# Optimization experiments

Measured on AMD Instinct MI355X. Metric: run time of the kernel, lower is better.

The kernel has to match this reference:

```python
import jax, jax.numpy as jnp
import numpy as np
from jax import lax

NVOX = 100
EPS = 1e-4
DN = ('NDHWC', 'DHWIO', 'NDHWC')

# scn semantics emulated densely: inactive voxels are identically zero and the
# active-site mask is re-applied after every layer, so submanifold convolution,
# strided sparse conv, sparse deconv and masked BN-ReLU compute the same values
# at active sites as SparseConvNet's rulebook gather-GEMM-scatter.

def _bnrelu(x, p, mask):
    # p: [4, C] = (gamma, beta, running_mean, running_var); inference-form BN.
    g, b, mu, v = p[0], p[1], p[2], p[3]
    return jax.nn.relu((x - mu) * (g * lax.rsqrt(v + EPS)) + b) * mask

def _subconv(x, w, mask):
    # Submanifold conv: inputs outside active set are zero; outputs only at active sites.
    return lax.conv_general_dilated(x, w, (1, 1, 1), 'SAME', dimension_numbers=DN) * mask

def _down(x, w):
    # scn.Convolution(dim, a, b, size=2, stride=2, bias=False)
    return lax.conv_general_dilated(x, w, (2, 2, 2), 'VALID', dimension_numbers=DN)

def _up(x, w, mask):
    # scn.Deconvolution restores the pre-downsample active set -> mask with finer mask.
    return lax.conv_transpose(x, w, (2, 2, 2), 'VALID', dimension_numbers=DN) * mask

def _pool_mask(mask):
    return lax.reduce_window(mask, 0.0, lax.max, (1, 2, 2, 2, 1), (1, 2, 2, 2, 1), 'VALID')

def _forward(coords, feats, w_in, w0a, wdown0, w1a, wdown1, w2, wup1, w1post, wup0, w0post,
             bnA, bnB, bnC, bnD, bnE, bnF, bnG, bnH, bnI, bnJ, linW, linb):
    i, j, k = coords[:, 0], coords[:, 1], coords[:, 2]
    # InputLayer mode=3: sum features at duplicate coordinates.
    grid = jnp.zeros((1, NVOX, NVOX, NVOX, 1), feats.dtype).at[0, i, j, k, 0].add(feats[:, 0])
    mask0 = jnp.zeros((1, NVOX, NVOX, NVOX, 1), feats.dtype).at[0, i, j, k, 0].set(1.0)
    mask1 = _pool_mask(mask0)   # 50^3 active set after strided conv
    mask2 = _pool_mask(mask1)   # 25^3

    x = _subconv(grid, w_in, mask0)                          # 1 -> 32
    x0 = _subconv(_bnrelu(x, bnA, mask0), w0a, mask0)        # level-0 VGG block
    d0 = _down(_bnrelu(x0, bnB, mask0), wdown0)              # 32 -> 64, 100 -> 50
    x1 = _subconv(_bnrelu(d0, bnC, mask1), w1a, mask1)       # level-1 VGG block
    d1 = _down(_bnrelu(x1, bnD, mask1), wdown1)              # 64 -> 96, 50 -> 25
    x2 = _subconv(_bnrelu(d1, bnE, mask2), w2, mask2)        # level-2 VGG block
    u1 = _up(_bnrelu(x2, bnF, mask2), wup1, mask1)           # 96 -> 64, 25 -> 50
    y1 = _subconv(_bnrelu(jnp.concatenate([x1, u1], -1), bnG, mask1), w1post, mask1)  # 128 -> 64
    u0 = _up(_bnrelu(y1, bnH, mask1), wup0, mask0)           # 64 -> 32, 50 -> 100
    y0 = _subconv(_bnrelu(jnp.concatenate([x0, u0], -1), bnI, mask0), w0post, mask0)  # 64 -> 32
    y = _bnrelu(y0, bnJ, mask0)                              # final BatchNormReLU(32)
    pts = y[0, i, j, k, :]                                   # OutputLayer: gather active sites [N,32]
    return pts @ linW + linb                                 # Linear(32, 3)


def setup_inputs() -> dict:
    key = jax.random.key(0)
    ks = jax.random.split(key, 24)
    N = 120000
    coords = jax.random.randint(ks[0], (N, 3), 0, NVOX, dtype=jnp.int32)
    feats = jax.random.normal(ks[1], (N, 1), jnp.float32)

    def w(k, shape, fan_in):
        return (jax.random.normal(k, shape, jnp.float32) / np.float32(np.sqrt(fan_in)))

    def bn(k, c):
        k1, k2, k3, k4 = jax.random.split(k, 4)
        return jnp.stack([
            1.0 + 0.1 * jax.random.normal(k1, (c,)),
            0.1 * jax.random.normal(k2, (c,)),
            0.1 * jax.random.normal(k3, (c,)),
            0.5 + jax.random.uniform(k4, (c,)),
        ]).astype(jnp.float32)

    return dict(
        coords=coords, feats=feats,
        w_in=w(ks[2], (3, 3, 3, 1, 32), 27),
        w0a=w(ks[3], (3, 3, 3, 32, 32), 27 * 32),
        wdown0=w(ks[4], (2, 2, 2, 32, 64), 8 * 32),
        w1a=w(ks[5], (3, 3, 3, 64, 64), 27 * 64),
        wdown1=w(ks[6], (2, 2, 2, 64, 96), 8 * 64),
        w2=w(ks[7], (3, 3, 3, 96, 96), 27 * 96),
        wup1=w(ks[8], (2, 2, 2, 96, 64), 96),
        w1post=w(ks[9], (3, 3, 3, 128, 64), 27 * 128),
        wup0=w(ks[10], (2, 2, 2, 64, 32), 64),
        w0post=w(ks[11], (3, 3, 3, 64, 32), 27 * 64),
        bnA=bn(ks[12], 32), bnB=bn(ks[13], 32), bnC=bn(ks[14], 64), bnD=bn(ks[15], 64),
        bnE=bn(ks[16], 96), bnF=bn(ks[17], 96), bnG=bn(ks[18], 128), bnH=bn(ks[19], 64),
        bnI=bn(ks[20], 64), bnJ=bn(ks[21], 32),
        linW=w(ks[22], (32, 3), 32),
        linb=0.01 * jax.random.normal(ks[23], (3,), jnp.float32),
    )


def reference(coords, feats, w_in, w0a, wdown0, w1a, wdown1, w2, wup1, w1post, wup0, w0post,
              bnA, bnB, bnC, bnD, bnE, bnF, bnG, bnH, bnI, bnJ, linW, linb):
    return _forward(coords, feats, w_in, w0a, wdown0, w1a, wdown1, w2, wup1, w1post, wup0, w0post,
                    bnA, bnB, bnC, bnD, bnE, bnF, bnG, bnH, bnI, bnJ, linW, linb)
```

## Files before the change

kernel.cpp:

```cpp
#include <hip/hip_runtime.h>


#define NVOX 100
#define EPSB 1e-4f
typedef unsigned long long u64;
typedef _Float16 h2 __attribute__((ext_vector_type(2)));
typedef _Float16 h8 __attribute__((ext_vector_type(8)));
typedef float f16v __attribute__((ext_vector_type(16)));
#define DEVFN __device__ __forceinline__

DEVFN float bnr(float v, float sc, float sh) { return fmaxf(fmaf(v, sc, sh), 0.f); }

template<int NTAPS, int CTOT, int COUT>
__global__ __launch_bounds__(256)
void prepB32(const float* __restrict__ w, h2* __restrict__ out)
{
    constexpr int CTG = COUT / 32, KCH = CTOT / 16;
    const int n = NTAPS * CTG * KCH * 256;
    const int idx = blockIdx.x * 256 + threadIdx.x;
    if (idx >= n) return;
    const int jh = idx & 3;
    const int lane = (idx >> 2) & 63;
    int r = idx >> 8;
    const int kc = r % KCH; r /= KCH;
    const int ct = r % CTG; const int t = r / CTG;
    const int k0 = kc * 16 + (lane >> 5) * 8 + 2 * jh;
    const int co = ct * 32 + (lane & 31);
    h2 v;
    v[0] = (_Float16)w[((size_t)t * CTOT + k0) * COUT + co];
    v[1] = (_Float16)w[((size_t)t * CTOT + k0 + 1) * COUT + co];
    out[idx] = v;
}

template<int EMODE, int COUT>
DEVFN void epilogue(float a, int srow, int ch,
                    float* outF, _Float16* o1, const float* sc1, const float* sh1,
                    _Float16* o2, const float* sc2, const float* sh2)
{
    if constexpr (EMODE == 0) {
        outF[(size_t)srow * COUT + ch] = a;
    } else if constexpr (EMODE == 3) {
        outF[(size_t)srow * COUT + ch] = bnr(a, sc1[ch], sh1[ch]);
    } else {
        o1[(size_t)srow * COUT + ch] = (_Float16)bnr(a, sc1[ch], sh1[ch]);
        if constexpr (EMODE == 2)
            o2[(size_t)srow * COUT + ch] = (_Float16)bnr(a, sc2[ch], sh2[ch]);
    }
}

template<int KC1, int KC2, int COUT, int S, int EMODE>
__global__ __launch_bounds__(64)
void gconv_m32(const h2* __restrict__ inA, const h2* __restrict__ inB,
               const h2* __restrict__ wb,
               const int* __restrict__ amap, const int* __restrict__ vlist,
               const int* __restrict__ cnt, int cap,
               float* __restrict__ outF, _Float16* __restrict__ o1,
               const float* __restrict__ sc1, const float* __restrict__ sh1,
               _Float16* __restrict__ o2,
               const float* __restrict__ sc2, const float* __restrict__ sh2)
{
    constexpr int KCH = KC1 + KC2;
    constexpr int CTG = COUT / 32;
    const int lane = threadIdx.x;
    const int cntv = *cnt;
    const int wbase = blockIdx.x * 32;
    if (wbase >= cntv) return;
    const int ct0 = blockIdx.y;
    const int l31 = lane & 31, ksub = lane >> 5;
    const int slot = wbase + l31;
    const bool on = slot < cntv;
    int X = 0, Y = 0, Z = 0;
    if (on) { const int v = vlist[slot]; X = v % S; const int r = v / S; Y = r % S; Z = r / S; }

    auto calc_ns = [&](int t) -> int {
        int ns = cap;
        if (on) {
            const int dz = t / 9 - 1, dy = (t / 3) % 3 - 1, dx = t % 3 - 1;
            const int nz = Z + dz, ny = Y + dy, nx = X + dx;
            if ((unsigned)nz < (unsigned)S && (unsigned)ny < (unsigned)S &&
                (unsigned)nx < (unsigned)S) {
                const int m = amap[(nz * S + ny) * S + nx];
                if (m >= 0) ns = m;
            }
        }
        return ns;
    };

    f16v acc = (f16v)(0.f);
    int ns = calc_ns(0);
#pragma unroll 1
    for (int t = 0; t < 27; ++t) {
        const int ns_nxt = (t + 1 < 27) ? calc_ns(t + 1) : cap;
        const h2* __restrict__ wt = wb + ((size_t)t * CTG + ct0) * KCH * 256;
#pragma unroll
        for (int kc = 0; kc < KC1; ++kc) {
            const h8 a = *reinterpret_cast<const h8*>(
                inA + (size_t)ns * (KC1 * 8) + kc * 8 + ksub * 4);
            const h8 b = *reinterpret_cast<const h8*>(
                wt + (size_t)kc * 256 + lane * 4);
            acc = __builtin_amdgcn_mfma_f32_32x32x16_f16(a, b, acc, 0, 0, 0);
        }
        if constexpr (KC2 > 0) {
#pragma unroll
            for (int kc = 0; kc < KC2; ++kc) {
                const h8 a = *reinterpret_cast<const h8*>(
                    inB + (size_t)ns * (KC2 * 8) + kc * 8 + ksub * 4);
                const h8 b = *reinterpret_cast<const h8*>(
                    wt + (size_t)(KC1 + kc) * 256 + lane * 4);
                acc = __builtin_amdgcn_mfma_f32_32x32x16_f16(a, b, acc, 0, 0, 0);
            }
        }
        ns = ns_nxt;
    }
    const int ch = ct0 * 32 + l31;
#pragma unroll
    for (int r = 0; r < 16; ++r) {
        const int row = (r & 3) + 8 * (r >> 2) + 4 * ksub;
        const int srow = wbase + row;
        if (srow < cntv)
            epilogue<EMODE, COUT>(acc[r], srow, ch, outF, o1, sc1, sh1, o2, sc2, sh2);
    }
}

template<int KCH, int COUT, int SC, int EMODE>
__global__ __launch_bounds__(64)
void dconv_m32(const h2* __restrict__ in, const h2* __restrict__ wb,
               const int* __restrict__ amap_f, const int* __restrict__ vlist_c,
               const int* __restrict__ cnt_c, int capf,
               float* __restrict__ outF, _Float16* __restrict__ o1,
               const float* __restrict__ sc1, const float* __restrict__ sh1)
{
    constexpr int SF = SC * 2;
    constexpr int CTG = COUT / 32;
    const int lane = threadIdx.x;
    const int cntv = *cnt_c;
    const int wbase = blockIdx.x * 32;
    if (wbase >= cntv) return;
    const int ct0 = blockIdx.y;
    const int l31 = lane & 31, ksub = lane >> 5;
    const int slot = wbase + l31;
    const bool on = slot < cntv;
    int X = 0, Y = 0, Z = 0;
    if (on) { const int v = vlist_c[slot]; X = v % SC; const int r = v / SC; Y = r % SC; Z = r / SC; }

    auto calc_ns = [&](int t) -> int {
        int ns = capf;
        if (on) {
            const int fz = 2 * Z + ((t >> 2) & 1);
            const int fy = 2 * Y + ((t >> 1) & 1);
            const int fx = 2 * X + (t & 1);
            const int m = amap_f[(fz * SF + fy) * SF + fx];
            if (m >= 0) ns = m;
        }
        return ns;
    };

    f16v acc = (f16v)(0.f);
    int ns = calc_ns(0);
#pragma unroll 1
    for (int t = 0; t < 8; ++t) {
        const int ns_nxt = (t + 1 < 8) ? calc_ns(t + 1) : capf;
        const h2* __restrict__ wt = wb + ((size_t)t * CTG + ct0) * KCH * 256;
#pragma unroll
        for (int kc = 0; kc < KCH; ++kc) {
            const h8 a = *reinterpret_cast<const h8*>(
                in + (size_t)ns * (KCH * 8) + kc * 8 + ksub * 4);
            const h8 b = *reinterpret_cast<const h8*>(
                wt + (size_t)kc * 256 + lane * 4);
            acc = __builtin_amdgcn_mfma_f32_32x32x16_f16(a, b, acc, 0, 0, 0);
        }
        ns = ns_nxt;
    }
    const int ch = ct0 * 32 + l31;
#pragma unroll
    for (int r = 0; r < 16; ++r) {
        const int row = (r & 3) + 8 * (r >> 2) + 4 * ksub;
        const int srow = wbase + row;
        if (srow < cntv)
            epilogue<EMODE, COUT>(acc[r], srow, ch, outF, o1, sc1, sh1,
                                  nullptr, nullptr, nullptr);
    }
}


template<int CTOT, int COUT>
DEVFN void stage_tap(const float* __restrict__ wtap, int cg32,
                     float* __restrict__ lbuf, int wid, int lane)
{
    constexpr int IPW = CTOT / 32;
#pragma unroll
    for (int i = 0; i < IPW; ++i) {
        const int chunk = wid * IPW + i;
        const int f4i = chunk * 64 + lane;
        const int ci = f4i >> 3, sub = f4i & 7;
        const float* g = wtap + ci * COUT + cg32 + sub * 4;
        __builtin_amdgcn_global_load_lds(
            (const __attribute__((address_space(1))) void*)g,
            (__attribute__((address_space(3))) void*)(lbuf + chunk * 256),
            16, 0, 0);
    }
}

template<int CIN>
DEVFN void dorow8(const float* __restrict__ row, const float* __restrict__ wl,
                  float (&acc)[8])
{
#pragma unroll 4
    for (int c0 = 0; c0 < CIN; c0 += 4) {
        const float4 a = *reinterpret_cast<const float4*>(row + c0);
        const float av[4] = {a.x, a.y, a.z, a.w};
#pragma unroll
        for (int j = 0; j < 4; ++j) {
            const float4 w0 = *reinterpret_cast<const float4*>(wl + (c0 + j) * 32);
            const float4 w1 = *reinterpret_cast<const float4*>(wl + (c0 + j) * 32 + 4);
            acc[0] = fmaf(av[j], w0.x, acc[0]);
            acc[1] = fmaf(av[j], w0.y, acc[1]);
            acc[2] = fmaf(av[j], w0.z, acc[2]);
            acc[3] = fmaf(av[j], w0.w, acc[3]);
            acc[4] = fmaf(av[j], w1.x, acc[4]);
            acc[5] = fmaf(av[j], w1.y, acc[5]);
            acc[6] = fmaf(av[j], w1.z, acc[6]);
            acc[7] = fmaf(av[j], w1.w, acc[7]);
        }
    }
}

template<int CIN, int COUT, int SC>
__global__ __launch_bounds__(256)
void uconv_w(const float* __restrict__ in, const float* __restrict__ w,
             const int* __restrict__ amap_f, const int* __restrict__ vlist_c,
             const int* __restrict__ cnt_c, _Float16* __restrict__ out,
             const float* __restrict__ sc, const float* __restrict__ sh)
{
    constexpr int SF = SC * 2;
    __shared__ float lw[2][CIN * 32];
    const int tid = threadIdx.x, lane = tid & 63, wid = tid >> 6;
    const int cntv = *cnt_c;
    if (blockIdx.x * 64 >= cntv) return;
    const int slot = blockIdx.x * 64 + lane;
    const int cg32 = blockIdx.y * 32;
    const bool on = slot < cntv;
    int X = 0, Y = 0, Z = 0;
    if (on) { const int v = vlist_c[slot]; X = v % SC; const int r = v / SC; Y = r % SC; Z = r / SC; }
    stage_tap<CIN, COUT>(w + (size_t)7 * CIN * COUT, cg32, lw[0], wid, lane);
    __syncthreads();
#pragma unroll 1
    for (int t = 0; t < 8; ++t) {
        if (t + 1 < 8)
            stage_tap<CIN, COUT>(w + (size_t)(6 - t) * CIN * COUT, cg32,
                                 lw[(t + 1) & 1], wid, lane);
        int cs = -1;
        if (on) {
            const int fz = 2 * Z + ((t >> 2) & 1);
            const int fy = 2 * Y + ((t >> 1) & 1);
            const int fx = 2 * X + (t & 1);
            cs = amap_f[(fz * SF + fy) * SF + fx];
        }
        if (cs >= 0) {
            float acc[8];
#pragma unroll
            for (int q = 0; q < 8; ++q) acc[q] = 0.f;
            dorow8<CIN>(in + (size_t)slot * CIN, &lw[t & 1][wid * 8], acc);
            union { float4 v[1]; _Float16 h[8]; } o;
            const int chb = cg32 + wid * 8;
#pragma unroll
            for (int q = 0; q < 8; ++q)
                o.h[q] = (_Float16)bnr(acc[q], sc[chb + q], sh[chb + q]);
            *reinterpret_cast<float4*>(out + (size_t)cs * COUT + chb) = o.v[0];
        }
        __syncthreads();
    }
}

template<int S>
__global__ __launch_bounds__(128)
void cin_k(const float* __restrict__ grid, const float* __restrict__ w,
           const int* __restrict__ vlist, const int* __restrict__ cnt,
           _Float16* __restrict__ out, const float* __restrict__ sc,
           const float* __restrict__ sh)
{
    const int wOff = __builtin_amdgcn_readfirstlane(threadIdx.x >> 6) * 16;
    const int slot = blockIdx.x * 64 + (threadIdx.x & 63);
    if (slot >= *cnt) return;
    const int v = vlist[slot];
    const int x = v % S;
    const int rem = v / S;
    const int y = rem % S;
    const int z = rem / S;
    float acc[16];
#pragma unroll
    for (int c = 0; c < 16; ++c) acc[c] = 0.f;
#pragma unroll
    for (int t = 0; t < 27; ++t) {
        const int dz = t / 9 - 1, dy = (t / 3) % 3 - 1, dx = t % 3 - 1;
        const int nz = z + dz, ny = y + dy, nx = x + dx;
        if ((unsigned)nz >= (unsigned)S || (unsigned)ny >= (unsigned)S ||
            (unsigned)nx >= (unsigned)S) continue;
        const float val = grid[(nz * S + ny) * S + nx];
        const float* __restrict__ wp = w + t * 32 + wOff;
#pragma unroll
        for (int c = 0; c < 16; ++c) acc[c] = fmaf(val, wp[c], acc[c]);
    }
    union { float4 v[2]; _Float16 h[16]; } o;
#pragma unroll
    for (int c = 0; c < 16; ++c)
        o.h[c] = (_Float16)bnr(acc[c], sc[wOff + c], sh[wOff + c]);
    float4* dst = reinterpret_cast<float4*>(out + (size_t)slot * 32 + wOff);
    dst[0] = o.v[0];
    dst[1] = o.v[1];
}

__global__ __launch_bounds__(256)
void final_k(const int* __restrict__ coords, const float* __restrict__ y0,
             const int* __restrict__ amap0, const float* __restrict__ ssJ,
             const float* __restrict__ linW, const float* __restrict__ linb,
             int N, float* __restrict__ outp)
{
    const int n = blockIdx.x * blockDim.x + threadIdx.x;
    if (n >= N) return;
    const int i = coords[3 * n + 0];
    const int j = coords[3 * n + 1];
    const int k = coords[3 * n + 2];
    const int v = (i * NVOX + j) * NVOX + k;
    const int s = amap0[v];
    float a0 = linb[0], a1 = linb[1], a2 = linb[2];
    if (s >= 0) {
        const float* __restrict__ row = y0 + (size_t)s * 32;
#pragma unroll
        for (int c = 0; c < 32; ++c) {
            const float t = bnr(row[c], ssJ[c], ssJ[32 + c]);
            a0 = fmaf(t, linW[c * 3 + 0], a0);
            a1 = fmaf(t, linW[c * 3 + 1], a1);
            a2 = fmaf(t, linW[c * 3 + 2], a2);
        }
    }
    outp[3 * n + 0] = a0;
    outp[3 * n + 1] = a1;
    outp[3 * n + 2] = a2;
}

__global__ void bn_prep(const float* __restrict__ A, const float* __restrict__ B,
                        const float* __restrict__ C, const float* __restrict__ D,
                        const float* __restrict__ E, const float* __restrict__ F,
                        const float* __restrict__ G, const float* __restrict__ H,
                        const float* __restrict__ I, const float* __restrict__ J,
                        float* __restrict__ ss)
{
    const float* bp[10] = {A, B, C, D, E, F, G, H, I, J};
    const int CH[10] = {32, 32, 64, 64, 96, 96, 128, 64, 64, 32};
    int idx = blockIdx.x * blockDim.x + threadIdx.x;
    if (idx >= 672) return;
    int l = 0, base = 0, off2 = 0;
    while (idx >= base + CH[l]) { base += CH[l]; off2 += 2 * CH[l]; ++l; }
    const int c = idx - base;
    const float* bn = bp[l];
    const int Cc = CH[l];
    const float g = bn[c], b = bn[Cc + c], mu = bn[2 * Cc + c], var = bn[3 * Cc + c];
    const float sc = g * rsqrtf(var + EPSB);
    ss[off2 + c] = sc;
    ss[off2 + Cc + c] = b - mu * sc;
}

__global__ __launch_bounds__(256)
void scatter_mark(const int* __restrict__ coords, const float* __restrict__ feats,
                  int N, float* __restrict__ grid, int* __restrict__ amap0)
{
    const int n = blockIdx.x * blockDim.x + threadIdx.x;
    if (n >= N) return;
    const int i = coords[3 * n + 0];
    const int j = coords[3 * n + 1];
    const int k = coords[3 * n + 2];
    const int v = (i * NVOX + j) * NVOX + k;
    atomicAdd(&grid[v], feats[n]);
    amap0[v] = -2;
}

template<int SC>
__global__ __launch_bounds__(256)
void flag_coarse(const int* __restrict__ amap_f, int* __restrict__ amap_c)
{
    constexpr int SF = SC * 2;
    const int v = blockIdx.x * blockDim.x + threadIdx.x;
    if (v >= SC * SC * SC) return;
    const int x = v % SC;
    const int rem = v / SC;
    const int y = rem % SC;
    const int z = rem / SC;
    bool any = false;
#pragma unroll
    for (int t = 0; t < 8; ++t) {
        const int fz = 2 * z + ((t >> 2) & 1);
        const int fy = 2 * y + ((t >> 1) & 1);
        const int fx = 2 * x + (t & 1);
        if (amap_f[(fz * SF + fy) * SF + fx] >= 0) any = true;
    }
    amap_c[v] = any ? -2 : -1;
}

__global__ __launch_bounds__(256)
void count_k(const int* __restrict__ flags, int V, int* __restrict__ counts)
{
    const int v = blockIdx.x * 256 + threadIdx.x;
    const bool act = (v < V) && (flags[v] == -2);
    const u64 m = __ballot(act);
    __shared__ int c[4];
    const int wid = threadIdx.x >> 6;
    if ((threadIdx.x & 63) == 0) c[wid] = __popcll(m);
    __syncthreads();
    if (threadIdx.x == 0) counts[blockIdx.x] = c[0] + c[1] + c[2] + c[3];
}

__global__ __launch_bounds__(1024)
void scan_k(int* __restrict__ counts, int nb, int* __restrict__ total)
{
    __shared__ int sums[1024];
    const int t = threadIdx.x;
    int v[4];
    int s = 0;
#pragma unroll
    for (int i = 0; i < 4; ++i) {
        const int idx = t * 4 + i;
        v[i] = (idx < nb) ? counts[idx] : 0;
        s += v[i];
    }
    sums[t] = s;
    __syncthreads();
    for (int d = 1; d < 1024; d <<= 1) {
        const int add = (t >= d) ? sums[t - d] : 0;
        __syncthreads();
        sums[t] += add;
        __syncthreads();
    }
    int base = (t > 0) ? sums[t - 1] : 0;
#pragma unroll
    for (int i = 0; i < 4; ++i) {
        const int idx = t * 4 + i;
        if (idx < nb) counts[idx] = base;
        base += v[i];
    }
    if (t == 1023) *total = sums[1023];
}

__global__ __launch_bounds__(256)
void emit_k(int* __restrict__ amap, int V, const int* __restrict__ offsets,
            int* __restrict__ vlist)
{
    const int v = blockIdx.x * 256 + threadIdx.x;
    const bool act = (v < V) && (amap[v] == -2);
    const u64 m = __ballot(act);
    __shared__ int wbase[4];
    const int wid = threadIdx.x >> 6;
    const int lane = threadIdx.x & 63;
    if (lane == 0) wbase[wid] = __popcll(m);
    __syncthreads();
    if (threadIdx.x == 0) {
        int s = 0;
#pragma unroll
        for (int i = 0; i < 4; ++i) { const int t = wbase[i]; wbase[i] = s; s += t; }
    }
    __syncthreads();
    if (act) {
        const int slot = offsets[blockIdx.x] + wbase[wid] +
                         __popcll(m & ((1ull << lane) - 1ull));
        amap[v] = slot;
        vlist[slot] = v;
    }
}

extern "C" void kernel_launch(void* const* d_in, const int* in_sizes, int n_in,
                              void* d_out, int out_size, void* d_ws, size_t ws_size,
                              hipStream_t stream) {
    const int*   coords = (const int*)d_in[0];
    const float* feats  = (const float*)d_in[1];
    const float* w_in   = (const float*)d_in[2];
    const float* w0a    = (const float*)d_in[3];
    const float* wdown0 = (const float*)d_in[4];
    const float* w1a    = (const float*)d_in[5];
    const float* wdown1 = (const float*)d_in[6];
    const float* w2     = (const float*)d_in[7];
    const float* wup1   = (const float*)d_in[8];
    const float* w1post = (const float*)d_in[9];
    const float* wup0   = (const float*)d_in[10];
    const float* w0post = (const float*)d_in[11];
    const float* linW = (const float*)d_in[22];
    const float* linb = (const float*)d_in[23];
    float* outp = (float*)d_out;

    const int N = in_sizes[1];
    const int V0 = NVOX * NVOX * NVOX;
    const int V1 = 50 * 50 * 50;
    const int V2 = 25 * 25 * 25;
    const int cap0 = N;
    const int cap1 = 100000;
    const int cap2 = V2;

    char* ws = (char*)d_ws;
    size_t off = 0;
    auto alloc = [&](size_t bytes) -> void* {
        void* p = ws + off;
        off += (bytes + 255) & ~(size_t)255;
        return p;
    };
    int*   amap0  = (int*)alloc((size_t)V0 * 4);
    int*   vlist0 = (int*)alloc((size_t)cap0 * 4);
    int*   amap1  = (int*)alloc((size_t)V1 * 4);
    int*   vlist1 = (int*)alloc((size_t)cap1 * 4);
    int*   amap2  = (int*)alloc((size_t)V2 * 4);
    int*   vlist2 = (int*)alloc((size_t)cap2 * 4);
    int*   cnt    = (int*)alloc(3 * 4);
    int*   counts = (int*)alloc(4096 * 4);
    float* ss     = (float*)alloc(1344 * 4);
    float* grid   = (float*)alloc((size_t)V0 * 4);
    _Float16* HA  = (_Float16*)alloc((size_t)(cap0 + 1) * 32 * 2);
    _Float16* HB  = (_Float16*)alloc((size_t)(cap0 + 1) * 32 * 2);
    _Float16* HI1 = (_Float16*)alloc((size_t)(cap0 + 1) * 32 * 2);
    _Float16* HI2 = (_Float16*)alloc((size_t)(cap0 + 1) * 32 * 2);
    _Float16* HC  = (_Float16*)alloc((size_t)(cap1 + 1) * 64 * 2);
    _Float16* HD  = (_Float16*)alloc((size_t)(cap1 + 1) * 64 * 2);
    _Float16* HG1 = (_Float16*)alloc((size_t)(cap1 + 1) * 64 * 2);
    _Float16* HG2 = (_Float16*)alloc((size_t)(cap1 + 1) * 64 * 2);
    _Float16* HE  = (_Float16*)alloc((size_t)(cap2 + 1) * 96 * 2);
    float* y0f  = (float*)alloc((size_t)cap0 * 32 * 4);
    float* actF = (float*)alloc((size_t)cap2 * 96 * 4);
    float* actH = (float*)alloc((size_t)cap1 * 64 * 4);
    h2* wbA  = (h2*)alloc((size_t)27 * 1 * 2 * 256 * 4);
    h2* wb1  = (h2*)alloc((size_t)27 * 2 * 4 * 256 * 4);
    h2* wb2  = (h2*)alloc((size_t)27 * 3 * 6 * 256 * 4);
    h2* wbP1 = (h2*)alloc((size_t)27 * 2 * 8 * 256 * 4);
    h2* wbP0 = (h2*)alloc((size_t)27 * 1 * 4 * 256 * 4);
    h2* wbD0 = (h2*)alloc((size_t)8 * 2 * 2 * 256 * 4);
    h2* wbD1 = (h2*)alloc((size_t)8 * 3 * 4 * 256 * 4);
    if (off > ws_size) return;

    const int B = 256;
    const int gN  = (N + B - 1) / B;
    const int nb0 = (V0 + B - 1) / B;
    const int nb1 = (V1 + B - 1) / B;
    const int nb2 = (V2 + B - 1) / B;
    const int sb0 = (cap0 + 63) / 64;
    const int sb1 = (cap1 + 63) / 64;
    const int sb2 = (cap2 + 63) / 64;
    const int g1w_0 = (cap0 + 31) / 32;
    const int g1w_1 = (cap1 + 31) / 32;
    const int g1w_2 = (cap2 + 31) / 32;

    hipMemsetAsync(amap0, 0xFF, (size_t)V0 * 4, stream);
    hipMemsetAsync(grid, 0, (size_t)V0 * 4, stream);
    hipMemsetAsync(HA + (size_t)cap0 * 32, 0, 64, stream);
    hipMemsetAsync(HB + (size_t)cap0 * 32, 0, 64, stream);
    hipMemsetAsync(HI1 + (size_t)cap0 * 32, 0, 64, stream);
    hipMemsetAsync(HI2 + (size_t)cap0 * 32, 0, 64, stream);
    hipMemsetAsync(HC + (size_t)cap1 * 64, 0, 128, stream);
    hipMemsetAsync(HD + (size_t)cap1 * 64, 0, 128, stream);
    hipMemsetAsync(HG1 + (size_t)cap1 * 64, 0, 128, stream);
    hipMemsetAsync(HG2 + (size_t)cap1 * 64, 0, 128, stream);
    hipMemsetAsync(HE + (size_t)cap2 * 96, 0, 192, stream);
    bn_prep<<<3, 256, 0, stream>>>((const float*)d_in[12], (const float*)d_in[13],
                                   (const float*)d_in[14], (const float*)d_in[15],
                                   (const float*)d_in[16], (const float*)d_in[17],
                                   (const float*)d_in[18], (const float*)d_in[19],
                                   (const float*)d_in[20], (const float*)d_in[21], ss);
    prepB32<27, 32, 32><<<(27 * 1 * 2 * 256 + 255) / 256, 256, 0, stream>>>(w0a, wbA);
    prepB32<27, 64, 64><<<(27 * 2 * 4 * 256 + 255) / 256, 256, 0, stream>>>(w1a, wb1);
    prepB32<27, 96, 96><<<(27 * 3 * 6 * 256 + 255) / 256, 256, 0, stream>>>(w2, wb2);
    prepB32<27, 128, 64><<<(27 * 2 * 8 * 256 + 255) / 256, 256, 0, stream>>>(w1post, wbP1);
    prepB32<27, 64, 32><<<(27 * 1 * 4 * 256 + 255) / 256, 256, 0, stream>>>(w0post, wbP0);
    prepB32<8, 32, 64><<<(8 * 2 * 2 * 256 + 255) / 256, 256, 0, stream>>>(wdown0, wbD0);
    prepB32<8, 64, 96><<<(8 * 3 * 4 * 256 + 255) / 256, 256, 0, stream>>>(wdown1, wbD1);
    scatter_mark<<<gN, B, 0, stream>>>(coords, feats, N, grid, amap0);
    count_k<<<nb0, B, 0, stream>>>(amap0, V0, counts);
    scan_k<<<1, 1024, 0, stream>>>(counts, nb0, cnt + 0);
    emit_k<<<nb0, B, 0, stream>>>(amap0, V0, counts, vlist0);
    flag_coarse<50><<<nb1, B, 0, stream>>>(amap0, amap1);
    count_k<<<nb1, B, 0, stream>>>(amap1, V1, counts);
    scan_k<<<1, 1024, 0, stream>>>(counts, nb1, cnt + 1);
    emit_k<<<nb1, B, 0, stream>>>(amap1, V1, counts, vlist1);
    flag_coarse<25><<<nb2, B, 0, stream>>>(amap1, amap2);
    count_k<<<nb2, B, 0, stream>>>(amap2, V2, counts);
    scan_k<<<1, 1024, 0, stream>>>(counts, nb2, cnt + 2);
    emit_k<<<nb2, B, 0, stream>>>(amap2, V2, counts, vlist2);

    cin_k<100><<<sb0, 128, 0, stream>>>(grid, w_in, vlist0, cnt + 0, HA,
                                        ss + 0, ss + 32);
    gconv_m32<2, 0, 32, 100, 2><<<dim3(g1w_0, 1), 64, 0, stream>>>(
        (const h2*)HA, nullptr, wbA, amap0, vlist0, cnt + 0, cap0,
        nullptr, HB, ss + 64, ss + 96, HI1, ss + 1152, ss + 1216);
    dconv_m32<2, 64, 50, 1><<<dim3(g1w_1, 2), 64, 0, stream>>>(
        (const h2*)HB, wbD0, amap0, vlist1, cnt + 1, cap0,
        nullptr, HC, ss + 128, ss + 192);
    gconv_m32<4, 0, 64, 50, 2><<<dim3(g1w_1, 2), 64, 0, stream>>>(
        (const h2*)HC, nullptr, wb1, amap1, vlist1, cnt + 1, cap1,
        nullptr, HD, ss + 256, ss + 320, HG1, ss + 768, ss + 896);
    dconv_m32<4, 96, 25, 1><<<dim3(g1w_2, 3), 64, 0, stream>>>(
        (const h2*)HD, wbD1, amap1, vlist2, cnt + 2, cap1,
        nullptr, HE, ss + 384, ss + 480);
    gconv_m32<6, 0, 96, 25, 3><<<dim3(g1w_2, 3), 64, 0, stream>>>(
        (const h2*)HE, nullptr, wb2, amap2, vlist2, cnt + 2, cap2,
        actF, nullptr, ss + 576, ss + 672, nullptr, nullptr, nullptr);
    uconv_w<96, 64, 25><<<dim3(sb2, 2), 256, 0, stream>>>(
        actF, wup1, amap1, vlist2, cnt + 2, HG2, ss + 768 + 64, ss + 896 + 64);
    gconv_m32<4, 4, 64, 50, 3><<<dim3(g1w_1, 2), 64, 0, stream>>>(
        (const h2*)HG1, (const h2*)HG2, wbP1, amap1, vlist1, cnt + 1, cap1,
        actH, nullptr, ss + 1024, ss + 1088, nullptr, nullptr, nullptr);
    uconv_w<64, 32, 50><<<dim3(sb1, 1), 256, 0, stream>>>(
        actH, wup0, amap0, vlist1, cnt + 1, HI2, ss + 1152 + 32, ss + 1216 + 32);
    gconv_m32<2, 2, 32, 100, 0><<<dim3(g1w_0, 1), 64, 0, stream>>>(
        (const h2*)HI1, (const h2*)HI2, wbP0, amap0, vlist0, cnt + 0, cap0,
        y0f, nullptr, nullptr, nullptr, nullptr, nullptr, nullptr);
    final_k<<<gN, B, 0, stream>>>(coords, y0f, amap0, ss + 1280, linW, linb, N, outp);
}
```

Baseline: 552.8 us.

## Compute multiple output-channel tiles per wave and swizzle blocks across XCDs

The gather-GEMM conv kernels gain a CTILES parameter, so one 64-thread wave can compute two 32-channel output tiles at 64-channel levels. Each gathered input fragment is then reused across both tiles instead of being re-gathered by a second block. Launches are flattened to 1D with an XCD-aware block-index remap, so consecutive logical blocks land on the same XCD for L2 locality. The cost is fewer waves and more accumulator registers per wave at the 64-channel levels, which may reduce latency hiding.

```diff
diff --git a/kernel.cpp b/kernel.cpp
--- a/kernel.cpp
+++ b/kernel.cpp
@@ -10,6 +10,13 @@
 #define DEVFN __device__ __forceinline__
 
 DEVFN float bnr(float v, float sc, float sh) { return fmaxf(fmaf(v, sc, sh), 0.f); }
+
+DEVFN int xcd_swz(int orig, int nwg)
+{
+    const int q = nwg >> 3, r = nwg & 7;
+    const int xcd = orig & 7, idx = orig >> 3;
+    return (xcd < r ? xcd * (q + 1) : r * (q + 1) + (xcd - r) * q) + idx;
+}
 
 template<int NTAPS, int CTOT, int COUT>
 __global__ __launch_bounds__(256)
@@ -48,12 +55,12 @@
     }
 }
 
-template<int KC1, int KC2, int COUT, int S, int EMODE>
+template<int KC1, int KC2, int CTILES, int COUT, int S, int EMODE>
 __global__ __launch_bounds__(64)
 void gconv_m32(const h2* __restrict__ inA, const h2* __restrict__ inB,
                const h2* __restrict__ wb,
                const int* __restrict__ amap, const int* __restrict__ vlist,
-               const int* __restrict__ cnt, int cap,
+               const int* __restrict__ cnt, int cap, int nbx,
                float* __restrict__ outF, _Float16* __restrict__ o1,
                const float* __restrict__ sc1, const float* __restrict__ sh1,
                _Float16* __restrict__ o2,
@@ -63,9 +70,10 @@
     constexpr int CTG = COUT / 32;
     const int lane = threadIdx.x;
     const int cntv = *cnt;
-    const int wbase = blockIdx.x * 32;
+    const int sid = xcd_swz(blockIdx.x, gridDim.x);
+    const int ct0 = sid / nbx;
+    const int wbase = (sid - ct0 * nbx) * 32;
     if (wbase >= cntv) return;
-    const int ct0 = blockIdx.y;
     const int l31 = lane & 31, ksub = lane >> 5;
     const int slot = wbase + l31;
     const bool on = slot < cntv;
@@ -86,47 +94,60 @@
         return ns;
     };
 
-    f16v acc = (f16v)(0.f);
+    f16v acc[CTILES];
+#pragma unroll
+    for (int c = 0; c < CTILES; ++c) acc[c] = (f16v)(0.f);
     int ns = calc_ns(0);
 #pragma unroll 1
     for (int t = 0; t < 27; ++t) {
         const int ns_nxt = (t + 1 < 27) ? calc_ns(t + 1) : cap;
-        const h2* __restrict__ wt = wb + ((size_t)t * CTG + ct0) * KCH * 256;
+        const h2* __restrict__ wt =
+            wb + ((size_t)t * CTG + ct0 * CTILES) * KCH * 256;
 #pragma unroll
         for (int kc = 0; kc < KC1; ++kc) {
             const h8 a = *reinterpret_cast<const h8*>(
                 inA + (size_t)ns * (KC1 * 8) + kc * 8 + ksub * 4);
-            const h8 b = *reinterpret_cast<const h8*>(
-                wt + (size_t)kc * 256 + lane * 4);
-            acc = __builtin_amdgcn_mfma_f32_32x32x16_f16(a, b, acc, 0, 0, 0);
+#pragma unroll
+            for (int ct = 0; ct < CTILES; ++ct) {
+                const h8 b = *reinterpret_cast<const h8*>(
+                    wt + ((size_t)ct * KCH + kc) * 256 + lane * 4);
+                acc[ct] = __builtin_amdgcn_mfma_f32_32x32x16_f16(a, b, acc[ct], 0, 0, 0);
+            }
         }
         if constexpr (KC2 > 0) {
 #pragma unroll
             for (int kc = 0; kc < KC2; ++kc) {
                 const h8 a = *reinterpret_cast<const h8*>(
                     inB + (size_t)ns * (KC2 * 8) + kc * 8 + ksub * 4);
-                const h8 b = *reinterpret_cast<const h8*>(
-                    wt + (size_t)(KC1 + kc) * 256 + lane * 4);
-                acc = __builtin_amdgcn_mfma_f32_32x32x16_f16(a, b, acc, 0, 0, 0);
+#pragma unroll
+                for (int ct = 0; ct < CTILES; ++ct) {
+                    const h8 b = *reinterpret_cast<const h8*>(
+                        wt + ((size_t)ct * KCH + KC1 + kc) * 256 + lane * 4);
+                    acc[ct] = __builtin_amdgcn_mfma_f32_32x32x16_f16(a, b, acc[ct], 0, 0, 0);
+                }
             }
         }
         ns = ns_nxt;
     }
-    const int ch = ct0 * 32 + l31;
-#pragma unroll
-    for (int r = 0; r < 16; ++r) {
-        const int row = (r & 3) + 8 * (r >> 2) + 4 * ksub;
-        const int srow = wbase + row;
-        if (srow < cntv)
-            epilogue<EMODE, COUT>(acc[r], srow, ch, outF, o1, sc1, sh1, o2, sc2, sh2);
-    }
-}
-
-template<int KCH, int COUT, int SC, int EMODE>
+#pragma unroll
+    for (int ct = 0; ct < CTILES; ++ct) {
+        const int ch = (ct0 * CTILES + ct) * 32 + l31;
+#pragma unroll
+        for (int r = 0; r < 16; ++r) {
+            const int row = (r & 3) + 8 * (r >> 2) + 4 * ksub;
+            const int srow = wbase + row;
+            if (srow < cntv)
+                epilogue<EMODE, COUT>(acc[ct][r], srow, ch, outF, o1, sc1, sh1,
+                                      o2, sc2, sh2);
+        }
+    }
+}
+
+template<int KCH, int CTILES, int COUT, int SC, int EMODE>
 __global__ __launch_bounds__(64)
 void dconv_m32(const h2* __restrict__ in, const h2* __restrict__ wb,
                const int* __restrict__ amap_f, const int* __restrict__ vlist_c,
-               const int* __restrict__ cnt_c, int capf,
+               const int* __restrict__ cnt_c, int capf, int nbx,
                float* __restrict__ outF, _Float16* __restrict__ o1,
                const float* __restrict__ sc1, const float* __restrict__ sh1)
 {
@@ -134,9 +155,10 @@
     constexpr int CTG = COUT / 32;
     const int lane = threadIdx.x;
     const int cntv = *cnt_c;
-    const int wbase = blockIdx.x * 32;
+    const int sid = xcd_swz(blockIdx.x, gridDim.x);
+    const int ct0 = sid / nbx;
+    const int wbase = (sid - ct0 * nbx) * 32;
     if (wbase >= cntv) return;
-    const int ct0 = blockIdx.y;
     const int l31 = lane & 31, ksub = lane >> 5;
     const int slot = wbase + l31;
     const bool on = slot < cntv;
@@ -155,30 +177,39 @@
         return ns;
     };
 
-    f16v acc = (f16v)(0.f);
+    f16v acc[CTILES];
+#pragma unroll
+    for (int c = 0; c < CTILES; ++c) acc[c] = (f16v)(0.f);
     int ns = calc_ns(0);
 #pragma unroll 1
     for (int t = 0; t < 8; ++t) {
         const int ns_nxt = (t + 1 < 8) ? calc_ns(t + 1) : capf;
-        const h2* __restrict__ wt = wb + ((size_t)t * CTG + ct0) * KCH * 256;
+        const h2* __restrict__ wt =
+            wb + ((size_t)t * CTG + ct0 * CTILES) * KCH * 256;
 #pragma unroll
         for (int kc = 0; kc < KCH; ++kc) {
             const h8 a = *reinterpret_cast<const h8*>(
                 in + (size_t)ns * (KCH * 8) + kc * 8 + ksub * 4);
-            const h8 b = *reinterpret_cast<const h8*>(
-                wt + (size_t)kc * 256 + lane * 4);
-            acc = __builtin_amdgcn_mfma_f32_32x32x16_f16(a, b, acc, 0, 0, 0);
+#pragma unroll
+            for (int ct = 0; ct < CTILES; ++ct) {
+                const h8 b = *reinterpret_cast<const h8*>(
+                    wt + ((size_t)ct * KCH + kc) * 256 + lane * 4);
+                acc[ct] = __builtin_amdgcn_mfma_f32_32x32x16_f16(a, b, acc[ct], 0, 0, 0);
+            }
         }
         ns = ns_nxt;
     }
-    const int ch = ct0 * 32 + l31;
-#pragma unroll
-    for (int r = 0; r < 16; ++r) {
-        const int row = (r & 3) + 8 * (r >> 2) + 4 * ksub;
-        const int srow = wbase + row;
-        if (srow < cntv)
-            epilogue<EMODE, COUT>(acc[r], srow, ch, outF, o1, sc1, sh1,
-                                  nullptr, nullptr, nullptr);
+#pragma unroll
+    for (int ct = 0; ct < CTILES; ++ct) {
+        const int ch = (ct0 * CTILES + ct) * 32 + l31;
+#pragma unroll
+        for (int r = 0; r < 16; ++r) {
+            const int row = (r & 3) + 8 * (r >> 2) + 4 * ksub;
+            const int srow = wbase + row;
+            if (srow < cntv)
+                epilogue<EMODE, COUT>(acc[ct][r], srow, ch, outF, o1, sc1, sh1,
+                                      nullptr, nullptr, nullptr);
+        }
     }
 }
 
@@ -582,30 +613,30 @@
 
     cin_k<100><<<sb0, 128, 0, stream>>>(grid, w_in, vlist0, cnt + 0, HA,
                                         ss + 0, ss + 32);
-    gconv_m32<2, 0, 32, 100, 2><<<dim3(g1w_0, 1), 64, 0, stream>>>(
-        (const h2*)HA, nullptr, wbA, amap0, vlist0, cnt + 0, cap0,
+    gconv_m32<2, 0, 1, 32, 100, 2><<<g1w_0, 64, 0, stream>>>(
+        (const h2*)HA, nullptr, wbA, amap0, vlist0, cnt + 0, cap0, g1w_0,
         nullptr, HB, ss + 64, ss + 96, HI1, ss + 1152, ss + 1216);
-    dconv_m32<2, 64, 50, 1><<<dim3(g1w_1, 2), 64, 0, stream>>>(
-        (const h2*)HB, wbD0, amap0, vlist1, cnt + 1, cap0,
+    dconv_m32<2, 2, 64, 50, 1><<<g1w_1, 64, 0, stream>>>(
+        (const h2*)HB, wbD0, amap0, vlist1, cnt + 1, cap0, g1w_1,
         nullptr, HC, ss + 128, ss + 192);
-    gconv_m32<4, 0, 64, 50, 2><<<dim3(g1w_1, 2), 64, 0, stream>>>(
-        (const h2*)HC, nullptr, wb1, amap1, vlist1, cnt + 1, cap1,
+    gconv_m32<4, 0, 2, 64, 50, 2><<<g1w_1, 64, 0, stream>>>(
+        (const h2*)HC, nullptr, wb1, amap1, vlist1, cnt + 1, cap1, g1w_1,
         nullptr, HD, ss + 256, ss + 320, HG1, ss + 768, ss + 896);
-    dconv_m32<4, 96, 25, 1><<<dim3(g1w_2, 3), 64, 0, stream>>>(
-        (const h2*)HD, wbD1, amap1, vlist2, cnt + 2, cap1,
+    dconv_m32<4, 1, 96, 25, 1><<<g1w_2 * 3, 64, 0, stream>>>(
+        (const h2*)HD, wbD1, amap1, vlist2, cnt + 2, cap1, g1w_2,
         nullptr, HE, ss + 384, ss + 480);
-    gconv_m32<6, 0, 96, 25, 3><<<dim3(g1w_2, 3), 64, 0, stream>>>(
-        (const h2*)HE, nullptr, wb2, amap2, vlist2, cnt + 2, cap2,
+    gconv_m32<6, 0, 1, 96, 25, 3><<<g1w_2 * 3, 64, 0, stream>>>(
+        (const h2*)HE, nullptr, wb2, amap2, vlist2, cnt + 2, cap2, g1w_2,
         actF, nullptr, ss + 576, ss + 672, nullptr, nullptr, nullptr);
     uconv_w<96, 64, 25><<<dim3(sb2, 2), 256, 0, stream>>>(
         actF, wup1, amap1, vlist2, cnt + 2, HG2, ss + 768 + 64, ss + 896 + 64);
-    gconv_m32<4, 4, 64, 50, 3><<<dim3(g1w_1, 2), 64, 0, stream>>>(
-        (const h2*)HG1, (const h2*)HG2, wbP1, amap1, vlist1, cnt + 1, cap1,
+    gconv_m32<4, 4, 2, 64, 50, 3><<<g1w_1, 64, 0, stream>>>(
+        (const h2*)HG1, (const h2*)HG2, wbP1, amap1, vlist1, cnt + 1, cap1, g1w_1,
         actH, nullptr, ss + 1024, ss + 1088, nullptr, nullptr, nullptr);
     uconv_w<64, 32, 50><<<dim3(sb1, 1), 256, 0, stream>>>(
         actH, wup0, amap0, vlist1, cnt + 1, HI2, ss + 1152 + 32, ss + 1216 + 32);
-    gconv_m32<2, 2, 32, 100, 0><<<dim3(g1w_0, 1), 64, 0, stream>>>(
-        (const h2*)HI1, (const h2*)HI2, wbP0, amap0, vlist0, cnt + 0, cap0,
+    gconv_m32<2, 2, 1, 32, 100, 0><<<g1w_0, 64, 0, stream>>>(
+        (const h2*)HI1, (const h2*)HI2, wbP0, amap0, vlist0, cnt + 0, cap0, g1w_0,
         y0f, nullptr, nullptr, nullptr, nullptr, nullptr, nullptr);
     final_k<<<gN, B, 0, stream>>>(coords, y0f, amap0, ss + 1280, linW, linb, N, outp);
 }
```

After: 516.6 us. -6.6%, faster.
